# Kernel optimization log

Hardware: AMD Instinct MI355X
Metric: run time of the kernel (lower is better)

Reference implementation:

```python
import jax, jax.numpy as jnp
import numpy as np

SCALE = 1.0

def setup_inputs() -> dict:
    key = jax.random.key(0)
    k1, k2 = jax.random.split(key)
    template = jax.random.normal(k1, (4, 8192, 3), dtype=jnp.float32)
    source = jax.random.normal(k2, (4, 8192, 3), dtype=jnp.float32)
    return {"template": template, "source": source}

def _chamfer(p0, p1):
    # p0: [B,N,3], p1: [B,M,3]
    # squared pairwise distances: [B,N,M]
    sq0 = jnp.sum(p0 * p0, axis=-1)  # [B,N]
    sq1 = jnp.sum(p1 * p1, axis=-1)  # [B,M]
    cross = jnp.einsum('bnd,bmd->bnm', p0, p1)
    d = sq0[:, :, None] + sq1[:, None, :] - 2.0 * cross  # [B,N,M]
    d = jnp.maximum(d, 0.0)
    cost_p0_p1 = jnp.min(d, axis=2)  # [B,N] min sq dist p0 -> p1
    cost_p1_p0 = jnp.min(d, axis=1)  # [B,M] min sq dist p1 -> p0
    c01 = jnp.mean(jnp.sqrt(cost_p0_p1), axis=-1)  # [B]
    c10 = jnp.mean(jnp.sqrt(cost_p1_p0), axis=-1)  # [B]
    return (c01 + c10) / 2.0  # [B]

def reference(template, source):
    p0 = template / SCALE
    p1 = source / SCALE
    per_batch = _chamfer(p0, p1)
    return jnp.mean(per_batch, axis=0)  # reduction='mean' -> scalar
```

## Files before the change

kernel.cpp:

```cpp
#include <hip/hip_runtime.h>
#include <math.h>

#define NPTS 8192
#define NB 4
#define BLK 256

typedef __attribute__((ext_vector_type(8))) short  short8v;
typedef __attribute__((ext_vector_type(16))) float f32x16;

__device__ __forceinline__ float min3f(float a, float b, float c) {
    float d;
    asm("v_min3_f32 %0, %1, %2, %3" : "=v"(d) : "v"(a), "v"(b), "v"(c));
    return d;
}
__device__ __forceinline__ unsigned short f2bf(float f) {
    unsigned u = __float_as_uint(f);
    return (unsigned short)((u + 0x7FFFu + ((u >> 16) & 1u)) >> 16);
}
__device__ __forceinline__ float bf2f(unsigned short h) {
    return __uint_as_float(((unsigned)h) << 16);
}

__global__ __launch_bounds__(BLK) void chamfer_pack(
    const float* __restrict__ tmpl, const float* __restrict__ src,
    short* __restrict__ apack, short* __restrict__ bpack)
{
    const int t   = blockIdx.x * BLK + threadIdx.x;
    const int arr = t >> 15;
    const int b   = (t >> 13) & 3;
    const int i   = t & (NPTS - 1);
    const float* p = (arr ? src : tmpl) + ((size_t)b * NPTS + i) * 3;
    const float x = p[0], y = p[1], z = p[2];

    const unsigned short xh = f2bf(x), yh = f2bf(y), zh = f2bf(z);
    const unsigned short xl = f2bf(x - bf2f(xh));
    const unsigned short yl = f2bf(y - bf2f(yh));
    const unsigned short zl = f2bf(z - bf2f(zh));
    const float w = fmaf(x, x, fmaf(y, y, z * z));
    const unsigned short wh = f2bf(w);
    const unsigned short wl = f2bf(w - bf2f(wh));
    const float mx = -2.f * x, my = -2.f * y, mz = -2.f * z;
    const unsigned short mxh = f2bf(mx), myh = f2bf(my), mzh = f2bf(mz);
    const unsigned short mxl = f2bf(mx - bf2f(mxh));
    const unsigned short myl = f2bf(my - bf2f(myh));
    const unsigned short mzl = f2bf(mz - bf2f(mzh));
    const unsigned short ONE = 0x3F80;

    const size_t base = (size_t)(arr * 4 + b) * (NPTS * 16);
    const int    tl   = i >> 5, lr = i & 31;
    short* ap = apack + base + (size_t)tl * 512;
    short* bp = bpack + base + (size_t)tl * 512;

    const short8v a0 = {(short)xh, (short)yh, (short)zh, (short)xl,
                        (short)yl, (short)zl, (short)xh, (short)yh};
    const short8v a1 = {(short)zh, (short)wh, (short)wl, 0, 0, 0, 0, 0};
    *(short8v*)(ap + lr * 8)        = a0;
    *(short8v*)(ap + (lr + 32) * 8) = a1;

    const short8v b0 = {(short)mxh, (short)myh, (short)mzh, (short)mxh,
                        (short)myh, (short)mzh, (short)mxl, (short)myl};
    const short8v b1 = {(short)mzl, (short)ONE, (short)ONE, 0, 0, 0, 0, 0};
    *(short8v*)(bp + lr * 8)        = b0;
    *(short8v*)(bp + (lr + 32) * 8) = b1;
}

__global__ __launch_bounds__(BLK) void chamfer_mfma(
    const short* __restrict__ apack, const short* __restrict__ bpack,
    float* __restrict__ partial)
{
    __shared__ __align__(16) short lds[2][8192];
    const int bd  = blockIdx.z;
    const int seg = blockIdx.y;
    const int qb  = blockIdx.x;
    const int b = bd >> 1, dir = bd & 1;
    const short* ab = apack + (size_t)((dir ^ 1) * 4 + b) * (NPTS * 16)
                            + (size_t)seg * 128 * 512;
    const short* bb = bpack + (size_t)(dir * 4 + b) * (NPTS * 16);
    const int tid = threadIdx.x, wid = tid >> 6, lane = tid & 63;

    const int qt = qb * 4 + wid;
    const short8v bfrag = *(const short8v*)(bb + (size_t)qt * 512 + lane * 8);

    float mn = 3.4e38f;
    short8v st[4];
#define LOADREGS(c) { const short* s_ = ab + (size_t)(c) * 8192;               \
    _Pragma("unroll") for (int i_ = 0; i_ < 4; i_++)                           \
        st[i_] = *(const short8v*)(s_ + i_ * 2048 + tid * 8); }
#define WRITEBUF(bf) { _Pragma("unroll") for (int i_ = 0; i_ < 4; i_++)        \
        *(short8v*)(&lds[bf][i_ * 2048 + tid * 8]) = st[i_]; }

    LOADREGS(0); WRITEBUF(0); LOADREGS(1);
    __syncthreads();
    for (int c = 0; c < 8; c++) {
        if (c + 1 < 8) WRITEBUF((c + 1) & 1);
        if (c + 2 < 8) LOADREGS(c + 2);
        const short* lbase = &lds[c & 1][lane * 8];
#pragma unroll
        for (int t = 0; t < 16; t++) {
            const short8v a = *(const short8v*)(lbase + t * 512);
            f32x16 d = __builtin_amdgcn_mfma_f32_32x32x16_bf16(
                a, bfrag, (f32x16)(0.f), 0, 0, 0);
            const float g0 = min3f(d[0],  d[1],  d[2]);
            const float g1 = min3f(d[3],  d[4],  d[5]);
            const float g2 = min3f(d[6],  d[7],  d[8]);
            const float g3 = min3f(d[9],  d[10], d[11]);
            const float g4 = min3f(d[12], d[13], d[14]);
            mn = min3f(mn, g0, g1);
            mn = min3f(mn, g2, g3);
            mn = min3f(mn, g4, d[15]);
        }
        __syncthreads();
    }
    mn = fminf(mn, __shfl_xor(mn, 32, 64));
    if (lane < 32)
        partial[((size_t)bd * 2 + seg) * NPTS + qt * 32 + lane] = mn;
}

__global__ __launch_bounds__(BLK) void chamfer_reduce(
    const float* __restrict__ tmpl, const float* __restrict__ src,
    const float* __restrict__ partial, float* __restrict__ out)
{
    const int t  = blockIdx.x * BLK + threadIdx.x;
    const int bd = t >> 13;
    const int qi = t & (NPTS - 1);
    const int b  = bd >> 1;
    const int dir = bd & 1;
    const float* qp = (dir ? src : tmpl) + (size_t)b * NPTS * 3;
    const float qx = qp[3 * qi + 0];
    const float qy = qp[3 * qi + 1];
    const float qz = qp[3 * qi + 2];
    const float sq = qx * qx + qy * qy + qz * qz;

    const float m = fminf(partial[((size_t)bd * 2 + 0) * NPTS + qi],
                          partial[((size_t)bd * 2 + 1) * NPTS + qi]);
    float v = sqrtf(fmaxf(sq + m, 0.f));

#pragma unroll
    for (int off = 32; off > 0; off >>= 1)
        v += __shfl_down(v, off, 64);

    __shared__ float wsum[BLK / 64];
    const int lane = threadIdx.x & 63;
    const int wid  = threadIdx.x >> 6;
    if (lane == 0) wsum[wid] = v;
    __syncthreads();
    if (threadIdx.x == 0) {
        float s = 0.f;
#pragma unroll
        for (int w = 0; w < BLK / 64; w++) s += wsum[w];
        atomicAdd(out, s * (1.0f / 65536.0f));
    }
}

extern "C" void kernel_launch(void* const* d_in, const int* in_sizes, int n_in,
                              void* d_out, int out_size, void* d_ws, size_t ws_size,
                              hipStream_t stream) {
    const float* tmpl = (const float*)d_in[0];
    const float* src  = (const float*)d_in[1];
    float* out = (float*)d_out;

    short* apack   = (short*)d_ws;
    short* bpack   = apack + (size_t)8 * NPTS * 16;
    float* partial = (float*)(bpack + (size_t)8 * NPTS * 16);

    hipMemsetAsync(d_out, 0, sizeof(float), stream);

    chamfer_pack<<<(2 * NB * NPTS) / BLK, BLK, 0, stream>>>(tmpl, src, apack, bpack);

    dim3 g1(NPTS / 128, 2, 2 * NB);
    chamfer_mfma<<<g1, BLK, 0, stream>>>(apack, bpack, partial);

    chamfer_reduce<<<(2 * NB * NPTS) / BLK, BLK, 0, stream>>>(tmpl, src, partial, out);
}
```

Baseline: 93.03 us.

## Give each wave two query tiles per LDS A-fragment and split source into four segments

```diff
diff --git a/kernel.cpp b/kernel.cpp
--- a/kernel.cpp
+++ b/kernel.cpp
@@ -4,6 +4,7 @@
 #define NPTS 8192
 #define NB 4
 #define BLK 256
+#define MSEG 4
 
 typedef __attribute__((ext_vector_type(8))) short  short8v;
 typedef __attribute__((ext_vector_type(16))) float f32x16;
@@ -23,8 +24,11 @@
 
 __global__ __launch_bounds__(BLK) void chamfer_pack(
     const float* __restrict__ tmpl, const float* __restrict__ src,
-    short* __restrict__ apack, short* __restrict__ bpack)
+    short* __restrict__ apack, short* __restrict__ bpack,
+    float* __restrict__ out)
 {
+    if (blockIdx.x == 0 && threadIdx.x == 0) out[0] = 0.f;
+
     const int t   = blockIdx.x * BLK + threadIdx.x;
     const int arr = t >> 15;
     const int b   = (t >> 13) & 3;
@@ -74,14 +78,15 @@
     const int qb  = blockIdx.x;
     const int b = bd >> 1, dir = bd & 1;
     const short* ab = apack + (size_t)((dir ^ 1) * 4 + b) * (NPTS * 16)
-                            + (size_t)seg * 128 * 512;
+                            + (size_t)seg * 64 * 512;
     const short* bb = bpack + (size_t)(dir * 4 + b) * (NPTS * 16);
     const int tid = threadIdx.x, wid = tid >> 6, lane = tid & 63;
 
-    const int qt = qb * 4 + wid;
-    const short8v bfrag = *(const short8v*)(bb + (size_t)qt * 512 + lane * 8);
+    const int qt0 = qb * 8 + wid * 2;
+    const short8v bf0 = *(const short8v*)(bb + (size_t)qt0 * 512 + lane * 8);
+    const short8v bf1 = *(const short8v*)(bb + (size_t)(qt0 + 1) * 512 + lane * 8);
 
-    float mn = 3.4e38f;
+    float mn0 = 3.4e38f, mn1 = 3.4e38f;
     short8v st[4];
 #define LOADREGS(c) { const short* s_ = ab + (size_t)(c) * 8192;               \
     _Pragma("unroll") for (int i_ = 0; i_ < 4; i_++)                           \
@@ -91,29 +96,47 @@
 
     LOADREGS(0); WRITEBUF(0); LOADREGS(1);
     __syncthreads();
-    for (int c = 0; c < 8; c++) {
-        if (c + 1 < 8) WRITEBUF((c + 1) & 1);
-        if (c + 2 < 8) LOADREGS(c + 2);
+    for (int c = 0; c < 4; c++) {
+        if (c + 1 < 4) WRITEBUF((c + 1) & 1);
+        if (c + 2 < 4) LOADREGS(c + 2);
         const short* lbase = &lds[c & 1][lane * 8];
 #pragma unroll
         for (int t = 0; t < 16; t++) {
             const short8v a = *(const short8v*)(lbase + t * 512);
-            f32x16 d = __builtin_amdgcn_mfma_f32_32x32x16_bf16(
-                a, bfrag, (f32x16)(0.f), 0, 0, 0);
-            const float g0 = min3f(d[0],  d[1],  d[2]);
-            const float g1 = min3f(d[3],  d[4],  d[5]);
-            const float g2 = min3f(d[6],  d[7],  d[8]);
-            const float g3 = min3f(d[9],  d[10], d[11]);
-            const float g4 = min3f(d[12], d[13], d[14]);
-            mn = min3f(mn, g0, g1);
-            mn = min3f(mn, g2, g3);
-            mn = min3f(mn, g4, d[15]);
+            f32x16 d0 = __builtin_amdgcn_mfma_f32_32x32x16_bf16(
+                a, bf0, (f32x16)(0.f), 0, 0, 0);
+            {
+                const float g0 = min3f(d0[0],  d0[1],  d0[2]);
+                const float g1 = min3f(d0[3],  d0[4],  d0[5]);
+                const float g2 = min3f(d0[6],  d0[7],  d0[8]);
+                const float g3 = min3f(d0[9],  d0[10], d0[11]);
+                const float g4 = min3f(d0[12], d0[13], d0[14]);
+                mn0 = min3f(mn0, g0, g1);
+                mn0 = min3f(mn0, g2, g3);
+                mn0 = min3f(mn0, g4, d0[15]);
+            }
+            f32x16 d1 = __builtin_amdgcn_mfma_f32_32x32x16_bf16(
+                a, bf1, (f32x16)(0.f), 0, 0, 0);
+            {
+                const float g0 = min3f(d1[0],  d1[1],  d1[2]);
+                const float g1 = min3f(d1[3],  d1[4],  d1[5]);
+                const float g2 = min3f(d1[6],  d1[7],  d1[8]);
+                const float g3 = min3f(d1[9],  d1[10], d1[11]);
+                const float g4 = min3f(d1[12], d1[13], d1[14]);
+                mn1 = min3f(mn1, g0, g1);
+                mn1 = min3f(mn1, g2, g3);
+                mn1 = min3f(mn1, g4, d1[15]);
+            }
         }
         __syncthreads();
     }
-    mn = fminf(mn, __shfl_xor(mn, 32, 64));
-    if (lane < 32)
-        partial[((size_t)bd * 2 + seg) * NPTS + qt * 32 + lane] = mn;
+    mn0 = fminf(mn0, __shfl_xor(mn0, 32, 64));
+    mn1 = fminf(mn1, __shfl_xor(mn1, 32, 64));
+    if (lane < 32) {
+        const size_t sb = ((size_t)bd * MSEG + seg) * NPTS;
+        partial[sb + qt0 * 32 + lane]       = mn0;
+        partial[sb + (qt0 + 1) * 32 + lane] = mn1;
+    }
 }
 
 __global__ __launch_bounds__(BLK) void chamfer_reduce(
@@ -131,8 +154,10 @@
     const float qz = qp[3 * qi + 2];
     const float sq = qx * qx + qy * qy + qz * qz;
 
-    const float m = fminf(partial[((size_t)bd * 2 + 0) * NPTS + qi],
-                          partial[((size_t)bd * 2 + 1) * NPTS + qi]);
+    float m = 3.4e38f;
+#pragma unroll
+    for (int s = 0; s < MSEG; s++)
+        m = fminf(m, partial[((size_t)bd * MSEG + s) * NPTS + qi]);
     float v = sqrtf(fmaxf(sq + m, 0.f));
 
 #pragma unroll
@@ -163,11 +188,9 @@
     short* bpack   = apack + (size_t)8 * NPTS * 16;
     float* partial = (float*)(bpack + (size_t)8 * NPTS * 16);
 
-    hipMemsetAsync(d_out, 0, sizeof(float), stream);
+    chamfer_pack<<<(2 * NB * NPTS) / BLK, BLK, 0, stream>>>(tmpl, src, apack, bpack, out);
 
-    chamfer_pack<<<(2 * NB * NPTS) / BLK, BLK, 0, stream>>>(tmpl, src, apack, bpack);
-
-    dim3 g1(NPTS / 128, 2, 2 * NB);
+    dim3 g1(32, MSEG, 2 * NB);
     chamfer_mfma<<<g1, BLK, 0, stream>>>(apack, bpack, partial);
 
     chamfer_reduce<<<(2 * NB * NPTS) / BLK, BLK, 0, stream>>>(tmpl, src, partial, out);
```

New measurement: 89.43 us. 1.04x faster.

## Register-block four query tiles per wave and split reference points into eight segments

Applied to the files above, without the earlier changes.

```diff
diff --git a/kernel.cpp b/kernel.cpp
--- a/kernel.cpp
+++ b/kernel.cpp
@@ -4,6 +4,8 @@
 #define NPTS 8192
 #define NB 4
 #define BLK 256
+#define MSEG 8
+#define QPW 4
 
 typedef __attribute__((ext_vector_type(8))) short  short8v;
 typedef __attribute__((ext_vector_type(16))) float f32x16;
@@ -23,8 +25,10 @@
 
 __global__ __launch_bounds__(BLK) void chamfer_pack(
     const float* __restrict__ tmpl, const float* __restrict__ src,
-    short* __restrict__ apack, short* __restrict__ bpack)
+    short* __restrict__ apack, float* __restrict__ out)
 {
+    if (blockIdx.x == 0 && threadIdx.x == 0) out[0] = 0.f;
+
     const int t   = blockIdx.x * BLK + threadIdx.x;
     const int arr = t >> 15;
     const int b   = (t >> 13) & 3;
@@ -39,33 +43,21 @@
     const float w = fmaf(x, x, fmaf(y, y, z * z));
     const unsigned short wh = f2bf(w);
     const unsigned short wl = f2bf(w - bf2f(wh));
-    const float mx = -2.f * x, my = -2.f * y, mz = -2.f * z;
-    const unsigned short mxh = f2bf(mx), myh = f2bf(my), mzh = f2bf(mz);
-    const unsigned short mxl = f2bf(mx - bf2f(mxh));
-    const unsigned short myl = f2bf(my - bf2f(myh));
-    const unsigned short mzl = f2bf(mz - bf2f(mzh));
-    const unsigned short ONE = 0x3F80;
 
     const size_t base = (size_t)(arr * 4 + b) * (NPTS * 16);
     const int    tl   = i >> 5, lr = i & 31;
     short* ap = apack + base + (size_t)tl * 512;
-    short* bp = bpack + base + (size_t)tl * 512;
 
     const short8v a0 = {(short)xh, (short)yh, (short)zh, (short)xl,
                         (short)yl, (short)zl, (short)xh, (short)yh};
     const short8v a1 = {(short)zh, (short)wh, (short)wl, 0, 0, 0, 0, 0};
     *(short8v*)(ap + lr * 8)        = a0;
     *(short8v*)(ap + (lr + 32) * 8) = a1;
-
-    const short8v b0 = {(short)mxh, (short)myh, (short)mzh, (short)mxh,
-                        (short)myh, (short)mzh, (short)mxl, (short)myl};
-    const short8v b1 = {(short)mzl, (short)ONE, (short)ONE, 0, 0, 0, 0, 0};
-    *(short8v*)(bp + lr * 8)        = b0;
-    *(short8v*)(bp + (lr + 32) * 8) = b1;
 }
 
 __global__ __launch_bounds__(BLK) void chamfer_mfma(
-    const short* __restrict__ apack, const short* __restrict__ bpack,
+    const short* __restrict__ apack,
+    const float* __restrict__ tmpl, const float* __restrict__ src,
     float* __restrict__ partial)
 {
     __shared__ __align__(16) short lds[2][8192];
@@ -74,46 +66,71 @@
     const int qb  = blockIdx.x;
     const int b = bd >> 1, dir = bd & 1;
     const short* ab = apack + (size_t)((dir ^ 1) * 4 + b) * (NPTS * 16)
-                            + (size_t)seg * 128 * 512;
-    const short* bb = bpack + (size_t)(dir * 4 + b) * (NPTS * 16);
+                            + (size_t)seg * 32 * 512;
+    const float* qp = (dir ? src : tmpl) + (size_t)b * NPTS * 3;
     const int tid = threadIdx.x, wid = tid >> 6, lane = tid & 63;
 
-    const int qt = qb * 4 + wid;
-    const short8v bfrag = *(const short8v*)(bb + (size_t)qt * 512 + lane * 8);
+    const int qt0 = qb * 16 + wid * QPW;
+    short8v bf[QPW];
+#pragma unroll
+    for (int p = 0; p < QPW; p++) {
+        const int qid = (qt0 + p) * 32 + (lane & 31);
+        const float x = qp[3 * qid], y = qp[3 * qid + 1], z = qp[3 * qid + 2];
+        const float mx = -2.f * x, my = -2.f * y, mz = -2.f * z;
+        const unsigned short mxh = f2bf(mx), myh = f2bf(my), mzh = f2bf(mz);
+        const unsigned short mxl = f2bf(mx - bf2f(mxh));
+        const unsigned short myl = f2bf(my - bf2f(myh));
+        const unsigned short mzl = f2bf(mz - bf2f(mzh));
+        const unsigned short ONE = 0x3F80;
+        const short8v b0 = {(short)mxh, (short)myh, (short)mzh, (short)mxh,
+                            (short)myh, (short)mzh, (short)mxl, (short)myl};
+        const short8v b1 = {(short)mzl, (short)ONE, (short)ONE, 0, 0, 0, 0, 0};
+        bf[p] = (lane < 32) ? b0 : b1;
+    }
 
-    float mn = 3.4e38f;
+    float mn[QPW];
+#pragma unroll
+    for (int p = 0; p < QPW; p++) mn[p] = 3.4e38f;
+
     short8v st[4];
 #define LOADREGS(c) { const short* s_ = ab + (size_t)(c) * 8192;               \
     _Pragma("unroll") for (int i_ = 0; i_ < 4; i_++)                           \
         st[i_] = *(const short8v*)(s_ + i_ * 2048 + tid * 8); }
-#define WRITEBUF(bf) { _Pragma("unroll") for (int i_ = 0; i_ < 4; i_++)        \
-        *(short8v*)(&lds[bf][i_ * 2048 + tid * 8]) = st[i_]; }
+#define WRITEBUF(bf_) { _Pragma("unroll") for (int i_ = 0; i_ < 4; i_++)       \
+        *(short8v*)(&lds[bf_][i_ * 2048 + tid * 8]) = st[i_]; }
 
     LOADREGS(0); WRITEBUF(0); LOADREGS(1);
     __syncthreads();
-    for (int c = 0; c < 8; c++) {
-        if (c + 1 < 8) WRITEBUF((c + 1) & 1);
-        if (c + 2 < 8) LOADREGS(c + 2);
-        const short* lbase = &lds[c & 1][lane * 8];
+    for (int c = 0; c < 2; c++) {
+        if (c == 0) WRITEBUF(1);
+        const short* lbase = &lds[c][lane * 8];
 #pragma unroll
         for (int t = 0; t < 16; t++) {
             const short8v a = *(const short8v*)(lbase + t * 512);
-            f32x16 d = __builtin_amdgcn_mfma_f32_32x32x16_bf16(
-                a, bfrag, (f32x16)(0.f), 0, 0, 0);
-            const float g0 = min3f(d[0],  d[1],  d[2]);
-            const float g1 = min3f(d[3],  d[4],  d[5]);
-            const float g2 = min3f(d[6],  d[7],  d[8]);
-            const float g3 = min3f(d[9],  d[10], d[11]);
-            const float g4 = min3f(d[12], d[13], d[14]);
-            mn = min3f(mn, g0, g1);
-            mn = min3f(mn, g2, g3);
-            mn = min3f(mn, g4, d[15]);
+#pragma unroll
+            for (int p = 0; p < QPW; p++) {
+                f32x16 d = __builtin_amdgcn_mfma_f32_32x32x16_bf16(
+                    a, bf[p], (f32x16)(0.f), 0, 0, 0);
+                const float g0 = min3f(d[0],  d[1],  d[2]);
+                const float g1 = min3f(d[3],  d[4],  d[5]);
+                const float g2 = min3f(d[6],  d[7],  d[8]);
+                const float g3 = min3f(d[9],  d[10], d[11]);
+                const float g4 = min3f(d[12], d[13], d[14]);
+                mn[p] = min3f(mn[p], g0, g1);
+                mn[p] = min3f(mn[p], g2, g3);
+                mn[p] = min3f(mn[p], g4, d[15]);
+            }
         }
-        __syncthreads();
+        if (c == 0) __syncthreads();
     }
-    mn = fminf(mn, __shfl_xor(mn, 32, 64));
-    if (lane < 32)
-        partial[((size_t)bd * 2 + seg) * NPTS + qt * 32 + lane] = mn;
+
+    const size_t sb = ((size_t)bd * MSEG + seg) * NPTS;
+#pragma unroll
+    for (int p = 0; p < QPW; p++) {
+        mn[p] = fminf(mn[p], __shfl_xor(mn[p], 32, 64));
+        if (lane < 32)
+            partial[sb + (size_t)(qt0 + p) * 32 + lane] = mn[p];
+    }
 }
 
 __global__ __launch_bounds__(BLK) void chamfer_reduce(
@@ -131,8 +148,10 @@
     const float qz = qp[3 * qi + 2];
     const float sq = qx * qx + qy * qy + qz * qz;
 
-    const float m = fminf(partial[((size_t)bd * 2 + 0) * NPTS + qi],
-                          partial[((size_t)bd * 2 + 1) * NPTS + qi]);
+    float m = 3.4e38f;
+#pragma unroll
+    for (int s = 0; s < MSEG; s++)
+        m = fminf(m, partial[((size_t)bd * MSEG + s) * NPTS + qi]);
     float v = sqrtf(fmaxf(sq + m, 0.f));
 
 #pragma unroll
@@ -160,15 +179,12 @@
     float* out = (float*)d_out;
 
     short* apack   = (short*)d_ws;
-    short* bpack   = apack + (size_t)8 * NPTS * 16;
-    float* partial = (float*)(bpack + (size_t)8 * NPTS * 16);
+    float* partial = (float*)(apack + (size_t)8 * NPTS * 16);
 
-    hipMemsetAsync(d_out, 0, sizeof(float), stream);
+    chamfer_pack<<<(2 * NB * NPTS) / BLK, BLK, 0, stream>>>(tmpl, src, apack, out);
 
-    chamfer_pack<<<(2 * NB * NPTS) / BLK, BLK, 0, stream>>>(tmpl, src, apack, bpack);
-
-    dim3 g1(NPTS / 128, 2, 2 * NB);
-    chamfer_mfma<<<g1, BLK, 0, stream>>>(apack, bpack, partial);
+    dim3 g1(16, MSEG, 2 * NB);
+    chamfer_mfma<<<g1, BLK, 0, stream>>>(apack, tmpl, src, partial);
 
     chamfer_reduce<<<(2 * NB * NPTS) / BLK, BLK, 0, stream>>>(tmpl, src, partial, out);
 }
```

Result: faster. 88.57 us (-4.8%).
